# Optimization experiments

Hardware: AMD Instinct MI355X
Metric: run time of the kernel (lower is better)

## Reference

```python
import jax, jax.numpy as jnp
import numpy as np

N = 100000      # nodes
E = 1250000     # edges
DIN = 128       # in_channels
H = 64          # hidden
DOUT = 40       # out_channels


def setup_inputs() -> dict:
    key = jax.random.key(0)
    k0, k1, k2, k3 = jax.random.split(key, 4)
    x = jax.random.normal(k0, (N, DIN), dtype=jnp.float32)
    edge_index = jax.random.randint(k1, (2, E), 0, N, dtype=jnp.int32)
    # glorot-style init for the GCNConv linear layers
    W1 = jax.random.normal(k2, (DIN, H), dtype=jnp.float32) * np.float32(1.0 / np.sqrt(DIN))
    b1 = jnp.zeros((H,), dtype=jnp.float32)
    W2 = jax.random.normal(k3, (H, DOUT), dtype=jnp.float32) * np.float32(1.0 / np.sqrt(H))
    b2 = jnp.zeros((DOUT,), dtype=jnp.float32)
    return {"x": x, "W1": W1, "b1": b1, "W2": W2, "b2": b2, "edge_index": edge_index}


def reference(x, W1, b1, W2, b2, edge_index):
    # GCN normalization with added self-loops (PyG GCNConv default):
    # norm_e = deg(dst)^-1/2 * deg(src)^-1/2
    loop = jnp.arange(N, dtype=edge_index.dtype)
    src = jnp.concatenate([edge_index[0], loop])
    dst = jnp.concatenate([edge_index[1], loop])
    deg = jax.ops.segment_sum(jnp.ones(src.shape[0], x.dtype), dst, num_segments=N)
    dinv = jax.lax.rsqrt(deg)  # deg >= 1 thanks to self-loops
    norm = dinv[src] * dinv[dst]  # [E+N]

    def gcn_conv(h, W, b):
        h = h @ W                                     # [N, d_out] linear (no bias)
        msg = h[src] * norm[:, None]                  # gather + normalize
        return jax.ops.segment_sum(msg, dst, num_segments=N) + b  # scatter-add + bias

    h = jax.nn.relu(gcn_conv(x, W1, b1))  # dropout p=0.0 -> identity
    return gcn_conv(h, W2, b2)
```

## Files before the change

kernel.cpp:

```cpp
#include <hip/hip_runtime.h>
#include <hip/hip_fp16.h>

#define NN   100000
#define EE   1250000
#define DIN  128
#define HID  64
#define DOUT 40

#define BN   512
#define NB   196
#define CH   4096
#define SEG  8192
#define SEG2 10240
#define S_BLKS 306
#define G_BLKS 1563

typedef _Float16 v8h __attribute__((ext_vector_type(8)));
typedef float    v4f __attribute__((ext_vector_type(4)));

__device__ __forceinline__ void acc8(const float4& v, float4& lo, float4& hi) {
    const __half2* hp = (const __half2*)&v;
    float2 f0 = __half22float2(hp[0]), f1 = __half22float2(hp[1]);
    float2 f2 = __half22float2(hp[2]), f3 = __half22float2(hp[3]);
    lo.x += f0.x; lo.y += f0.y; lo.z += f1.x; lo.w += f1.y;
    hi.x += f2.x; hi.y += f2.y; hi.z += f3.x; hi.w += f3.y;
}

__device__ __forceinline__ void sthalf8(__half* p, const float4& lo, const float4& hi, float d) {
    float4 st;
    __half2* hp = (__half2*)&st;
    hp[0] = __floats2half2_rn(lo.x * d, lo.y * d);
    hp[1] = __floats2half2_rn(lo.z * d, lo.w * d);
    hp[2] = __floats2half2_rn(hi.x * d, hi.y * d);
    hp[3] = __floats2half2_rn(hi.z * d, hi.w * d);
    *(float4*)p = st;
}

__global__ __launch_bounds__(256) void k_wprep(const float* __restrict__ W1,
                                               const float* __restrict__ W2,
                                               __half* __restrict__ w1frag,
                                               __half* __restrict__ w2frag,
                                               int* __restrict__ bucket_fill,
                                               __half* __restrict__ xw1h,
                                               __half* __restrict__ hw2p) {
    int t = threadIdx.x;
    if (blockIdx.x == 5 && t < NB) bucket_fill[t] = 0;
    if (blockIdx.x == 0 && t < 13) {
        float4 z = make_float4(0.f, 0.f, 0.f, 0.f);
        if (t < 8) ((float4*)(xw1h + (size_t)NN * HID))[t] = z;
        else       ((float4*)(hw2p + (size_t)NN * 40))[t - 8] = z;
    }
    int e = blockIdx.x * 256 + t;
    if (e < 1024) {
        int ct = e >> 8, ki = (e >> 6) & 3, l = e & 63;
        int q = l >> 4, n = l & 15;
        v8h o;
        #pragma unroll
        for (int j = 0; j < 8; ++j)
            o[j] = (_Float16)W1[(ki * 32 + q * 8 + j) * 64 + ct * 16 + n];
        ((v8h*)w1frag)[e] = o;
    } else {
        int e2 = e - 1024;
        if (e2 < 384) {
            int ct = e2 >> 7, ki = (e2 >> 6) & 1, l = e2 & 63;
            int q = l >> 4, n = l & 15;
            int col = ct * 16 + n;
            v8h o;
            #pragma unroll
            for (int j = 0; j < 8; ++j)
                o[j] = (col < DOUT) ? (_Float16)W2[(ki * 32 + q * 8 + j) * DOUT + col]
                                    : (_Float16)0.0f;
            ((v8h*)w2frag)[e2] = o;
        }
    }
}

__global__ __launch_bounds__(256) void k_fat(const int* __restrict__ src,
                                             const int* __restrict__ dst,
                                             int* __restrict__ bucket_fill,
                                             int* __restrict__ ebuf,
                                             const float* __restrict__ x,
                                             const __half* __restrict__ w1frag,
                                             __half* __restrict__ xw1h) {
    __shared__ int smem[4096];
    int t = threadIdx.x;
    if (blockIdx.x < S_BLKS) {
        int* hist  = smem;
        int* gbase = smem + 256;
        int* rcur  = smem + 512;
        for (int i = t; i < NB; i += 256) { hist[i] = 0; rcur[i] = 0; }
        __syncthreads();
        int e0 = blockIdx.x * CH;
        int ep[16], eb[16];
        #pragma unroll
        for (int j = 0; j < 16; ++j) {
            int e = e0 + j * 256 + t;
            bool valid = (e < EE);
            if (valid) {
                int dd_ = dst[e];
                ep[j] = (src[e] << 9) | (dd_ & 511);
                eb[j] = dd_ >> 9;
                atomicAdd(&hist[eb[j]], 1);
            } else {
                ep[j] = 0; eb[j] = -1;
            }
        }
        __syncthreads();
        for (int i = t; i < NB; i += 256)
            gbase[i] = atomicAdd(&bucket_fill[i], hist[i]);
        __syncthreads();
        #pragma unroll
        for (int j = 0; j < 16; ++j) {
            if (eb[j] >= 0) {
                int r = atomicAdd(&rcur[eb[j]], 1);
                ebuf[eb[j] * SEG + gbase[eb[j]] + r] = ep[j];
            }
        }
    } else {
        float4* sb4 = (float4*)smem;
        const float4* wf = (const float4*)w1frag;
        #pragma unroll
        for (int i = 0; i < 4; ++i) sb4[t + i * 256] = wf[t + i * 256];
        __syncthreads();
        const v8h* sbh = (const v8h*)sb4;
        int wv = t >> 6, l = t & 63;
        int q = l >> 4, n = l & 15;
        int row0 = (blockIdx.x - S_BLKS) * 64 + wv * 16;
        int m = row0 + n;
        bool mv = (m < NN);
        const float* xr = x + (size_t)(mv ? m : 0) * DIN + q * 8;
        v8h afrag[4];
        #pragma unroll
        for (int ki = 0; ki < 4; ++ki) {
            float4 u0 = mv ? ((const float4*)(xr + ki * 32))[0] : make_float4(0.f,0.f,0.f,0.f);
            float4 u1 = mv ? ((const float4*)(xr + ki * 32))[1] : make_float4(0.f,0.f,0.f,0.f);
            v8h a;
            a[0] = (_Float16)u0.x; a[1] = (_Float16)u0.y;
            a[2] = (_Float16)u0.z; a[3] = (_Float16)u0.w;
            a[4] = (_Float16)u1.x; a[5] = (_Float16)u1.y;
            a[6] = (_Float16)u1.z; a[7] = (_Float16)u1.w;
            afrag[ki] = a;
        }
        v4f acc[4];
        #pragma unroll
        for (int ct = 0; ct < 4; ++ct) acc[ct] = (v4f){0.f, 0.f, 0.f, 0.f};
        #pragma unroll
        for (int ct = 0; ct < 4; ++ct) {
            #pragma unroll
            for (int ki = 0; ki < 4; ++ki)
                acc[ct] = __builtin_amdgcn_mfma_f32_16x16x32_f16(
                    afrag[ki], sbh[(ct * 4 + ki) * 64 + l], acc[ct], 0, 0, 0);
        }
        _Float16* outh = (_Float16*)xw1h;
        #pragma unroll
        for (int r = 0; r < 4; ++r) {
            int rr = row0 + q * 4 + r;
            if (rr < NN) {
                #pragma unroll
                for (int ct = 0; ct < 4; ++ct)
                    outh[(size_t)rr * HID + ct * 16 + n] = (_Float16)acc[ct][r];
            }
        }
    }
}

__global__ __launch_bounds__(512) void kB_csr(const int* __restrict__ ebuf,
                                              const int* __restrict__ bucket_fill,
                                              int* __restrict__ pofs,
                                              float* __restrict__ dinv,
                                              int* __restrict__ esrc,
                                              __half* __restrict__ xw1h) {
    __shared__ int lcnt[BN], sAa[BN], sBb[BN], lcur[BN];
    int t = threadIdx.x;
    int b = blockIdx.x;
    int eb0 = b * SEG;
    int eb2 = b * SEG2;
    int ecnt = bucket_fill[b];
    lcnt[t] = 0;
    __syncthreads();
    for (int j = t; j < ecnt; j += 512)
        atomicAdd(&lcnt[ebuf[eb0 + j] & 511], 1);
    __syncthreads();
    int cnt  = lcnt[t];
    int pcnt = (cnt + 7) & ~7;
    sAa[t] = pcnt;
    __syncthreads();
    int* s = sAa; int* d = sBb;
    for (int off = 1; off < BN; off <<= 1) {
        d[t] = s[t] + ((t >= off) ? s[t - off] : 0);
        __syncthreads();
        int* tmp = s; s = d; d = tmp;
    }
    int base_node = b * BN;
    int excl = s[t] - pcnt;
    lcur[t] = excl;
    int node = base_node + t;
    if (node < NN) {
        pofs[node] = ((eb2 + excl) << 10) | pcnt;
        dinv[node] = rsqrtf((float)cnt + 1.0f);
    }
    for (int i = t; i < SEG2; i += 512) esrc[eb2 + i] = NN;
    __syncthreads();
    for (int j = t; j < ecnt; j += 512) {
        int p = ebuf[eb0 + j];
        int r = atomicAdd(&lcur[p & 511], 1);
        esrc[eb2 + r] = p >> 9;
    }
    float4* xr4 = (float4*)xw1h;
    for (int i = t; i < BN * 8; i += 512) {
        int li = i >> 3;
        int node2 = base_node + li;
        if (node2 < NN) {
            float di = rsqrtf((float)lcnt[li] + 1.0f);
            float4 v = xr4[(size_t)node2 * 8 + (i & 7)];
            __half2* h = (__half2*)&v;
            #pragma unroll
            for (int u = 0; u < 4; ++u) {
                float2 f = __half22float2(h[u]);
                h[u] = __floats2half2_rn(f.x * di, f.y * di);
            }
            xr4[(size_t)node2 * 8 + (i & 7)] = v;
        }
    }
}

__global__ __launch_bounds__(256, 8) void k_fuse(const __half* __restrict__ xw1h,
                                                 const float* __restrict__ dinv,
                                                 const int* __restrict__ pofs,
                                                 const int* __restrict__ esrc,
                                                 const float* __restrict__ b1,
                                                 const __half* __restrict__ w2frag,
                                                 __half* __restrict__ hw2p) {
    __shared__ __half sh[32 * 72];
    __shared__ float4 sb4[384];
    __shared__ float sb1[64];
    int t = threadIdx.x;
    const float4* wf = (const float4*)w2frag;
    if (t < 192) { sb4[t] = wf[t]; sb4[t + 192] = wf[t + 192]; }
    if (t >= 192) sb1[t - 192] = b1[t - 192];

    int d0 = blockIdx.x * 32;
    int g = t >> 3, q = t & 7;
    int dd = d0 + g;
    const float4* tab4 = (const float4*)xw1h;
    float4 tl = make_float4(0.f,0.f,0.f,0.f), th = make_float4(0.f,0.f,0.f,0.f);
    acc8(tab4[(size_t)dd * 8 + q], tl, th);
    int p_ = pofs[dd];
    int j = p_ >> 10;
    int n8 = (p_ & 1023) >> 3;
    for (int m = 0; m < n8; ++m, j += 8) {
        int e[8];
        float4 v[8];
        #pragma unroll
        for (int u = 0; u < 8; ++u) e[u] = esrc[j + u];
        #pragma unroll
        for (int u = 0; u < 8; ++u) v[u] = tab4[(size_t)e[u] * 8 + q];
        #pragma unroll
        for (int u = 0; u < 8; ++u) acc8(v[u], tl, th);
    }
    sthalf8(sh + g * 72 + q * 8, tl, th, dinv[dd]);
    __syncthreads();

    int wv = t >> 6, l = t & 63;
    if (wv < 2) {
        const v8h* sbh = (const v8h*)sb4;
        int qq = l >> 4, n = l & 15;
        int srow = wv * 16 + n;
        v8h afrag[2];
        #pragma unroll
        for (int ki = 0; ki < 2; ++ki) {
            v8h a = *(const v8h*)(sh + srow * 72 + ki * 32 + qq * 8);
            #pragma unroll
            for (int jj = 0; jj < 8; ++jj) {
                float av = (float)a[jj] + sb1[ki * 32 + qq * 8 + jj];
                a[jj] = (_Float16)fmaxf(av, 0.f);
            }
            afrag[ki] = a;
        }
        v4f acc[3];
        #pragma unroll
        for (int ct = 0; ct < 3; ++ct) acc[ct] = (v4f){0.f, 0.f, 0.f, 0.f};
        #pragma unroll
        for (int ct = 0; ct < 3; ++ct) {
            #pragma unroll
            for (int ki = 0; ki < 2; ++ki)
                acc[ct] = __builtin_amdgcn_mfma_f32_16x16x32_f16(
                    afrag[ki], sbh[(ct * 2 + ki) * 64 + l], acc[ct], 0, 0, 0);
        }
        _Float16* outh = (_Float16*)hw2p;
        #pragma unroll
        for (int r = 0; r < 4; ++r) {
            int rr = d0 + wv * 16 + qq * 4 + r;
            float di = dinv[rr];
            outh[(size_t)rr * 40 + n]      = (_Float16)(acc[0][r] * di);
            outh[(size_t)rr * 40 + 16 + n] = (_Float16)(acc[1][r] * di);
            if (n < 8)
                outh[(size_t)rr * 40 + 32 + n] = (_Float16)(acc[2][r] * di);
        }
    }
}

__global__ __launch_bounds__(256, 8) void k_agg2(const __half* __restrict__ hw2p,
                                                 const float* __restrict__ dinv,
                                                 const int* __restrict__ pofs,
                                                 const int* __restrict__ esrc,
                                                 const float* __restrict__ b2,
                                                 float* __restrict__ out) {
    int t = threadIdx.x;
    int g = t >> 3, q = t & 7;
    int qc = (q < 5) ? q : (q - 3);
    int dd = blockIdx.x * 32 + g;
    const float4* tab4 = (const float4*)hw2p;
    float4 tl = make_float4(0.f,0.f,0.f,0.f), th = make_float4(0.f,0.f,0.f,0.f);
    acc8(tab4[(size_t)dd * 5 + qc], tl, th);
    int p_ = pofs[dd];
    int j = p_ >> 10;
    int n8 = (p_ & 1023) >> 3;
    for (int m = 0; m < n8; ++m, j += 8) {
        int e[8];
        float4 v[8];
        #pragma unroll
        for (int u = 0; u < 8; ++u) e[u] = esrc[j + u];
        #pragma unroll
        for (int u = 0; u < 8; ++u) v[u] = tab4[(size_t)e[u] * 5 + qc];
        #pragma unroll
        for (int u = 0; u < 8; ++u) acc8(v[u], tl, th);
    }
    if (q < 5) {
        float di = dinv[dd];
        const float4* b24 = (const float4*)(b2 + q * 8);
        float4 c0 = b24[0], c1 = b24[1];
        float* op = out + (size_t)dd * DOUT + q * 8;
        ((float4*)op)[0] = make_float4(tl.x * di + c0.x, tl.y * di + c0.y,
                                       tl.z * di + c0.z, tl.w * di + c0.w);
        ((float4*)op)[1] = make_float4(th.x * di + c1.x, th.y * di + c1.y,
                                       th.z * di + c1.z, th.w * di + c1.w);
    }
}

extern "C" void kernel_launch(void* const* d_in, const int* in_sizes, int n_in,
                              void* d_out, int out_size, void* d_ws, size_t ws_size,
                              hipStream_t stream) {
    const float* x  = (const float*)d_in[0];
    const float* W1 = (const float*)d_in[1];
    const float* b1 = (const float*)d_in[2];
    const float* W2 = (const float*)d_in[3];
    const float* b2 = (const float*)d_in[4];
    const int*   ei = (const int*)d_in[5];
    const int* src = ei;
    const int* dst = ei + EE;
    float* out = (float*)d_out;

    float* ws = (float*)d_ws;
    int*    bucket_fill = (int*)ws;
    int*    pofs        = (int*)ws + 256;
    float*  dinv        = ws + 100352;
    int*    ebuf        = (int*)ws + 200704;
    int*    esrc        = (int*)ws + 1806336;
    __half* xw1h        = (__half*)(ws + 3813376);
    __half* hw2p        = (__half*)(ws + 7013408);
    __half* w1frag      = (__half*)(ws + 9013428);
    __half* w2frag      = (__half*)(ws + 9017524);

    k_wprep <<<6, 256, 0, stream>>>(W1, W2, w1frag, w2frag, bucket_fill, xw1h, hw2p);
    k_fat   <<<S_BLKS + G_BLKS, 256, 0, stream>>>(src, dst, bucket_fill, ebuf, x, w1frag, xw1h);
    kB_csr  <<<NB, 512, 0, stream>>>(ebuf, bucket_fill, pofs, dinv, esrc, xw1h);
    k_fuse  <<<NN / 32, 256, 0, stream>>>(xw1h, dinv, pofs, esrc, b1, w2frag, hw2p);
    k_agg2  <<<NN / 32, 256, 0, stream>>>(hw2p, dinv, pofs, esrc, b2, out);
}
```

Measured before the change: 182.1 us.

## Sort destination nodes by degree within buckets to balance aggregation warps

Inside the CSR build kernel, nodes in each 512-node bucket are counting-sorted by degree into a permutation array. The fused layer-1 kernel and the layer-2 aggregation kernel then process nodes in that order, so the 8-thread groups sharing a wave have similar edge counts and less divergent loop trip counts. The esrc padding fill now writes only each node's pad slots instead of the whole segment. This adds an indirection load, and scattered output row writes replace contiguous ones.

```diff
diff --git a/kernel.cpp b/kernel.cpp
--- a/kernel.cpp
+++ b/kernel.cpp
@@ -169,14 +169,17 @@
                                               int* __restrict__ pofs,
                                               float* __restrict__ dinv,
                                               int* __restrict__ esrc,
-                                              __half* __restrict__ xw1h) {
+                                              __half* __restrict__ xw1h,
+                                              int* __restrict__ bperm) {
     __shared__ int lcnt[BN], sAa[BN], sBb[BN], lcur[BN];
+    __shared__ int hbin[64];
     int t = threadIdx.x;
     int b = blockIdx.x;
     int eb0 = b * SEG;
     int eb2 = b * SEG2;
     int ecnt = bucket_fill[b];
     lcnt[t] = 0;
+    if (t < 64) hbin[t] = 0;
     __syncthreads();
     for (int j = t; j < ecnt; j += 512)
         atomicAdd(&lcnt[ebuf[eb0 + j] & 511], 1);
@@ -184,22 +187,34 @@
     int cnt  = lcnt[t];
     int pcnt = (cnt + 7) & ~7;
     sAa[t] = pcnt;
-    __syncthreads();
+    int base_node = b * BN;
+    int node = base_node + t;
+    bool real = (node < NN);
+    int key = min(cnt, 63);
+    if (real) atomicAdd(&hbin[key], 1);
+    __syncthreads();
+    if (t == 0) {
+        int run = 0;
+        for (int i = 0; i < 64; ++i) { int c = hbin[i]; hbin[i] = run; run += c; }
+    }
+    __syncthreads();
+    if (real) {
+        int r = atomicAdd(&hbin[key], 1);
+        bperm[base_node + r] = node;
+    }
     int* s = sAa; int* d = sBb;
     for (int off = 1; off < BN; off <<= 1) {
         d[t] = s[t] + ((t >= off) ? s[t - off] : 0);
         __syncthreads();
         int* tmp = s; s = d; d = tmp;
     }
-    int base_node = b * BN;
     int excl = s[t] - pcnt;
     lcur[t] = excl;
-    int node = base_node + t;
-    if (node < NN) {
+    if (real) {
         pofs[node] = ((eb2 + excl) << 10) | pcnt;
         dinv[node] = rsqrtf((float)cnt + 1.0f);
     }
-    for (int i = t; i < SEG2; i += 512) esrc[eb2 + i] = NN;
+    for (int i = excl + cnt; i < excl + pcnt; ++i) esrc[eb2 + i] = NN;
     __syncthreads();
     for (int j = t; j < ecnt; j += 512) {
         int p = ebuf[eb0 + j];
@@ -230,7 +245,8 @@
                                                  const int* __restrict__ esrc,
                                                  const float* __restrict__ b1,
                                                  const __half* __restrict__ w2frag,
-                                                 __half* __restrict__ hw2p) {
+                                                 __half* __restrict__ hw2p,
+                                                 const int* __restrict__ bperm) {
     __shared__ __half sh[32 * 72];
     __shared__ float4 sb4[384];
     __shared__ float sb1[64];
@@ -241,7 +257,7 @@
 
     int d0 = blockIdx.x * 32;
     int g = t >> 3, q = t & 7;
-    int dd = d0 + g;
+    int dd = bperm[d0 + g];
     const float4* tab4 = (const float4*)xw1h;
     float4 tl = make_float4(0.f,0.f,0.f,0.f), th = make_float4(0.f,0.f,0.f,0.f);
     acc8(tab4[(size_t)dd * 8 + q], tl, th);
@@ -290,7 +306,8 @@
         _Float16* outh = (_Float16*)hw2p;
         #pragma unroll
         for (int r = 0; r < 4; ++r) {
-            int rr = d0 + wv * 16 + qq * 4 + r;
+            int slot = d0 + wv * 16 + qq * 4 + r;
+            int rr = bperm[slot];
             float di = dinv[rr];
             outh[(size_t)rr * 40 + n]      = (_Float16)(acc[0][r] * di);
             outh[(size_t)rr * 40 + 16 + n] = (_Float16)(acc[1][r] * di);
@@ -305,11 +322,12 @@
                                                  const int* __restrict__ pofs,
                                                  const int* __restrict__ esrc,
                                                  const float* __restrict__ b2,
-                                                 float* __restrict__ out) {
+                                                 float* __restrict__ out,
+                                                 const int* __restrict__ bperm) {
     int t = threadIdx.x;
     int g = t >> 3, q = t & 7;
     int qc = (q < 5) ? q : (q - 3);
-    int dd = blockIdx.x * 32 + g;
+    int dd = bperm[blockIdx.x * 32 + g];
     const float4* tab4 = (const float4*)hw2p;
     float4 tl = make_float4(0.f,0.f,0.f,0.f), th = make_float4(0.f,0.f,0.f,0.f);
     acc8(tab4[(size_t)dd * 5 + qc], tl, th);
@@ -361,10 +379,11 @@
     __half* hw2p        = (__half*)(ws + 7013408);
     __half* w1frag      = (__half*)(ws + 9013428);
     __half* w2frag      = (__half*)(ws + 9017524);
+    int*    bperm       = (int*)ws + 9019060;
 
     k_wprep <<<6, 256, 0, stream>>>(W1, W2, w1frag, w2frag, bucket_fill, xw1h, hw2p);
     k_fat   <<<S_BLKS + G_BLKS, 256, 0, stream>>>(src, dst, bucket_fill, ebuf, x, w1frag, xw1h);
-    kB_csr  <<<NB, 512, 0, stream>>>(ebuf, bucket_fill, pofs, dinv, esrc, xw1h);
-    k_fuse  <<<NN / 32, 256, 0, stream>>>(xw1h, dinv, pofs, esrc, b1, w2frag, hw2p);
-    k_agg2  <<<NN / 32, 256, 0, stream>>>(hw2p, dinv, pofs, esrc, b2, out);
-}
+    kB_csr  <<<NB, 512, 0, stream>>>(ebuf, bucket_fill, pofs, dinv, esrc, xw1h, bperm);
+    k_fuse  <<<NN / 32, 256, 0, stream>>>(xw1h, dinv, pofs, esrc, b1, w2frag, hw2p, bperm);
+    k_agg2  <<<NN / 32, 256, 0, stream>>>(hw2p, dinv, pofs, esrc, b2, out, bperm);
+}
```

After: 201.1 us. +10.5%, slower.
